# Kernel optimization log

Hardware: AMD Instinct MI355X
Metric: run time of the kernel (lower is better)

Reference implementation:

```python
import jax, jax.numpy as jnp
import numpy as np

N_USERS = 50000
N_ITEMS = 30000
N_ENT = 100000
N_REL = 11          # relations are 1..10; table has N_REL-1 rows
E = 500000          # KG triplets
EI = 1000000        # user-item interaction edges
D = 64              # emb_size (must equal 2*KD for router input)
KD = 32             # FactSemanticEmbedding embedding_dim (complex half-dim)
HID = 64            # GatingRouter hidden (channel)
HOPS = 3            # context_hops
NTH = 3             # hop_threshold N
GAMMA = 0.2


def setup_inputs() -> dict:
    key = jax.random.key(0)
    ks = jax.random.split(key, 24)
    g = lambda i, shape, s=0.1: (jax.random.normal(ks[i], shape) * s).astype(jnp.float32)
    return dict(
        user_embed=g(0, (N_USERS, D)), item_embed=g(1, (N_ITEMS, D)),
        Wq=g(2, (D, D)), Wk=g(3, (D, D)), Wv=g(4, (D, D)),
        ent_real=g(5, (N_ENT, KD)), ent_imag=g(6, (N_ENT, KD)),
        rel_real=g(7, (N_REL - 1, KD)), rel_imag=g(8, (N_REL - 1, KD)),
        fp_W1=g(9, (6 * KD, 2 * KD)), fp_b1=jnp.zeros((2 * KD,), jnp.float32),
        fp_W2=g(10, (2 * KD, 3)), fp_b2=jnp.zeros((3,), jnp.float32),
        rt_W1=g(11, (D, HID)), rt_b1=jnp.zeros((HID,), jnp.float32),
        rt_W2=g(12, (HID, D)), rt_b2=jnp.zeros((D,), jnp.float32),
        relation_emb=g(13, (N_REL - 1, D)),
        user_emb=g(14, (N_USERS, D)), entity_emb=g(15, (N_ENT, D)),
        inter_edge_w=jax.random.uniform(ks[16], (EI,), jnp.float32),
        edge_index=jax.random.randint(ks[17], (2, E), 0, N_ENT),
        edge_type=jax.random.randint(ks[18], (E,), 1, N_REL),
        inter_edge=jnp.stack([jax.random.randint(ks[19], (EI,), 0, N_USERS),
                              jax.random.randint(ks[20], (EI,), 0, N_ITEMS)]),
    )


def _normalize(x):  # F.normalize(dim=-1, eps=1e-8)
    n = jnp.linalg.norm(x, axis=-1, keepdims=True)
    return x / jnp.maximum(n, 1e-8)


def _n2n(x):
    return jnp.nan_to_num(x, nan=0.0, posinf=1e4, neginf=1e-4)


def reference(user_embed, item_embed, Wq, Wk, Wv, ent_real, ent_imag, rel_real,
              rel_imag, fp_W1, fp_b1, fp_W2, fp_b2, rt_W1, rt_b1, rt_W2, rt_b2,
              relation_emb, user_emb, entity_emb, inter_edge_w,
              edge_index, edge_type, inter_edge):
    users, items = inter_edge[0], inter_edge[1]
    # --- AttentionPreferenceMiner (dropout off / eval) ---
    q = (user_embed @ Wq)[users]           # [EI, D]
    k = (item_embed @ Wk)[items]
    v = (item_embed @ Wv)[items]
    scores = (q * k).sum(-1) / jnp.sqrt(jnp.float32(D)) * inter_edge_w
    m = jax.ops.segment_max(scores, users, num_segments=N_USERS)
    ex = jnp.exp(scores - m[users])
    den = jax.ops.segment_sum(ex, users, num_segments=N_USERS)
    alpha = ex / den[users]                # scatter_softmax over users
    cnt_u = jax.ops.segment_sum(jnp.ones_like(scores), users, num_segments=N_USERS)
    user_pref = jax.ops.segment_sum(v * alpha[:, None], users, num_segments=N_USERS)
    user_pref = user_pref / jnp.maximum(cnt_u, 1.0)[:, None]   # scatter_mean
    # --- FactSemanticEmbedding ---
    h, t = edge_index[0], edge_index[1]
    r = edge_type - 1
    hr, hi = ent_real[h], ent_imag[h]
    rr, ri = rel_real[r], rel_imag[r]
    tr, ti = ent_real[t], ent_imag[t]
    feat = jnp.concatenate([hr, hi, rr, ri, tr, ti], axis=-1)  # [E, 6*KD]
    w = jax.nn.softmax(jax.nn.sigmoid(feat @ fp_W1 + fp_b1) @ fp_W2 + fp_b2, axis=-1)
    br = w[:, 0:1] * hr + w[:, 1:2] * rr + w[:, 2:3] * tr
    bi = w[:, 0:1] * hi + w[:, 1:2] * ri + w[:, 2:3] * ti
    fact = jnp.concatenate([br, bi], axis=1)                   # [E, D]
    # --- GatingRouter: sum_j (aligned @ pref^T)[i,j] == aligned @ pref.sum(0) ---
    aligned = jax.nn.sigmoid(fact @ rt_W1 + rt_b1) @ rt_W2 + rt_b2
    omega = (aligned @ user_pref.sum(0)) / jnp.sqrt(jnp.float32(HID))  # [E]
    # --- GraphConv (mess_dropout off) ---
    rel_e = relation_emb[r]                                    # [E, D]
    cnt_h = jax.ops.segment_sum(jnp.ones((E,), omega.dtype), h, num_segments=N_ENT)
    seg_o = jax.ops.segment_sum(omega, h, num_segments=E)      # dim_size=omega.shape[0]
    alpha_g = omega / (seg_o[h] + 1e-8)
    eta = jnp.where(alpha_g > GAMMA, alpha_g, 0.0)
    seg_e = jax.ops.segment_sum(eta, h, num_segments=E)
    eta = eta / (seg_e[h] + 1e-8)
    e_emb, u_emb = entity_emb, user_emb
    ent_res, usr_res = entity_emb, user_emb
    for hop in range(1, HOPS + 1):
        neigh = e_emb[t] * rel_e
        rho = alpha_g if hop < NTH else eta
        e_agg = jax.ops.segment_sum(rho[:, None] * neigh, h, num_segments=N_ENT)
        e_agg = e_agg / jnp.maximum(cnt_h, 1.0)[:, None]       # scatter_mean
        item_agg = inter_edge_w[:, None] * e_emb[items]
        u_agg = jax.ops.segment_sum(item_agg, users, num_segments=N_USERS)
        e_emb = _n2n(_normalize(e_agg))
        u_emb = _n2n(_normalize(u_agg))
        ent_res = ent_res + e_emb
        usr_res = usr_res + u_emb
    return jnp.concatenate([ent_res, usr_res], axis=0)        # [N_ENT+N_USERS, D]
```

## Files before the change

### kernel.cpp

```cpp
#include <hip/hip_runtime.h>
#include <hip/hip_bf16.h>
#include <math.h>

#define N_USERS 50000
#define N_ITEMS 30000
#define N_ENT   100000
#define NE      500000
#define NEI     1000000
#define D       64
#define GAMMA   0.2f

#define UBK ((N_USERS + 255) / 256)
#define HBK ((N_ENT + 255) / 256)
#define PCHUNK 4096

typedef __hip_bfloat16 bf16;

__device__ __forceinline__ float wave_sum(float v) {
    #pragma unroll
    for (int off = 32; off > 0; off >>= 1) v += __shfl_xor(v, off, 64);
    return v;
}

__device__ __forceinline__ float g16_sum(float v) {
    #pragma unroll
    for (int off = 1; off < 16; off <<= 1) v += __shfl_xor(v, off, 64);
    return v;
}

__device__ __forceinline__ float bits2f(unsigned short u) {
    return __uint_as_float(((unsigned)u) << 16);
}

__device__ __forceinline__ unsigned short f2bf_bits(float f) {
    bf16 b = __float2bfloat16(f);
    return *(unsigned short*)&b;
}

__device__ __forceinline__ float sigmoidf(float x) {
    return __fdividef(1.0f, 1.0f + __expf(-x));
}

__device__ __forceinline__ float n2n(float y) {
    if (isnan(y)) return 0.0f;
    if (isinf(y)) return y > 0.0f ? 1e4f : 1e-4f;
    return y;
}

__global__ __launch_bounds__(256) void k_histb(const int* __restrict__ ie,
        const int* __restrict__ eidx, int* __restrict__ bcntU,
        int* __restrict__ bcntH, int UCH) {
    __shared__ int lc[HBK + 1];
    int t = threadIdx.x;
    int b = blockIdx.x;
    for (int i = t; i < HBK + 1; i += 256) lc[i] = 0;
    __syncthreads();
    if (b < UCH) {
        int base = b * PCHUNK;
        #pragma unroll
        for (int i = 0; i < PCHUNK / 256; i++) {
            int e = base + i * 256 + t;
            if (e < NEI) atomicAdd(&lc[ie[e] >> 8], 1);
        }
        __syncthreads();
        for (int i = t; i < UBK; i += 256) if (lc[i]) atomicAdd(&bcntU[i], lc[i]);
    } else {
        int base = (b - UCH) * PCHUNK;
        #pragma unroll
        for (int i = 0; i < PCHUNK / 256; i++) {
            int e = base + i * 256 + t;
            if (e < NE) atomicAdd(&lc[eidx[e] >> 8], 1);
        }
        __syncthreads();
        for (int i = t; i < HBK; i += 256) if (lc[i]) atomicAdd(&bcntH[i], lc[i]);
    }
}

__global__ void k_scanb(const int* __restrict__ bcntU, int* __restrict__ bOffU,
                        int* __restrict__ bcurU, const int* __restrict__ bcntH,
                        int* __restrict__ bOffH, int* __restrict__ bcurH,
                        int* __restrict__ offU, int* __restrict__ offH) {
    __shared__ int sh[512];
    int t = threadIdx.x;
    const int* c; int* o; int* cu; int n; int tot;
    if (blockIdx.x == 0) { c = bcntU; o = bOffU; cu = bcurU; n = UBK; tot = NEI; }
    else                 { c = bcntH; o = bOffH; cu = bcurH; n = HBK; tot = NE; }
    int v = (t < n) ? c[t] : 0;
    sh[t] = v;
    __syncthreads();
    for (int d = 1; d < 512; d <<= 1) {
        int x = (t >= d) ? sh[t - d] : 0;
        __syncthreads();
        sh[t] += x;
        __syncthreads();
    }
    if (t < n) { int ex = sh[t] - v; o[t] = ex; cu[t] = ex; }
    if (t == 0) {
        o[n] = tot;
        if (blockIdx.x == 0) offU[N_USERS] = NEI;
        else                 offH[N_ENT] = NE;
    }
}

__global__ __launch_bounds__(256) void k_part1(const int* __restrict__ ie,
        const float* __restrict__ w, const int* __restrict__ eidx,
        const int* __restrict__ etype, int* __restrict__ bcurU,
        int* __restrict__ bcurH, int2* __restrict__ stIW,
        int* __restrict__ stTR, int UCH) {
    __shared__ int lcnt[HBK + 1];
    __shared__ int lbase[HBK + 1];
    int t = threadIdx.x;
    int b = blockIdx.x;
    for (int i = t; i < HBK + 1; i += 256) lcnt[i] = 0;
    __syncthreads();
    if (b < UCH) {
        int base = b * PCHUNK;
        int bkt[PCHUNK / 256], rnk[PCHUNK / 256];
        #pragma unroll
        for (int i = 0; i < PCHUNK / 256; i++) {
            int e = base + i * 256 + t;
            bkt[i] = -1;
            rnk[i] = 0;
            if (e < NEI) {
                int k = ie[e] >> 8;
                bkt[i] = k;
                rnk[i] = atomicAdd(&lcnt[k], 1);
            }
        }
        __syncthreads();
        for (int i = t; i < UBK; i += 256)
            if (lcnt[i] > 0) lbase[i] = atomicAdd(&bcurU[i], lcnt[i]);
        __syncthreads();
        #pragma unroll
        for (int i = 0; i < PCHUNK / 256; i++) {
            int e = base + i * 256 + t;
            if (bkt[i] >= 0) {
                int pos = lbase[bkt[i]] + rnk[i];
                int ul = ie[e] & 255;
                stIW[pos] = make_int2(ie[NEI + e] | (ul << 24), __float_as_int(w[e]));
            }
        }
    } else {
        int base = (b - UCH) * PCHUNK;
        int bkt[PCHUNK / 256], rnk[PCHUNK / 256];
        #pragma unroll
        for (int i = 0; i < PCHUNK / 256; i++) {
            int e = base + i * 256 + t;
            bkt[i] = -1;
            rnk[i] = 0;
            if (e < NE) {
                int k = eidx[e] >> 8;
                bkt[i] = k;
                rnk[i] = atomicAdd(&lcnt[k], 1);
            }
        }
        __syncthreads();
        for (int i = t; i < HBK; i += 256)
            if (lcnt[i] > 0) lbase[i] = atomicAdd(&bcurH[i], lcnt[i]);
        __syncthreads();
        #pragma unroll
        for (int i = 0; i < PCHUNK / 256; i++) {
            int e = base + i * 256 + t;
            if (bkt[i] >= 0) {
                int pos = lbase[bkt[i]] + rnk[i];
                int hl = eidx[e] & 255;
                stTR[pos] = eidx[NE + e] | ((etype[e] - 1) << 20) | (hl << 24);
            }
        }
    }
}

__global__ __launch_bounds__(256) void k_part2(const int* __restrict__ bOffU,
        const int2* __restrict__ stIW, int* __restrict__ offU,
        int2* __restrict__ csr_itw, const int* __restrict__ bOffH,
        const int* __restrict__ stTR, int* __restrict__ offH,
        int* __restrict__ csr_tr, int UBKc) {
    __shared__ int lcnt[256];
    __shared__ int lcur[256];
    int t = threadIdx.x;
    int b = blockIdx.x;
    lcnt[t] = 0;
    __syncthreads();
    if (b < UBKc) {
        int s = bOffU[b], e = bOffU[b + 1];
        for (int j = s + t; j < e; j += 256)
            atomicAdd(&lcnt[((unsigned)stIW[j].x) >> 24], 1);
        __syncthreads();
        int v = lcnt[t];
        lcur[t] = v;
        __syncthreads();
        for (int d = 1; d < 256; d <<= 1) {
            int x = (t >= d) ? lcur[t - d] : 0;
            __syncthreads();
            lcur[t] += x;
            __syncthreads();
        }
        int base = s + lcur[t] - v;
        int u = (b << 8) + t;
        if (u < N_USERS) offU[u] = base;
        __syncthreads();
        lcur[t] = base;
        __syncthreads();
        for (int j = s + t; j < e; j += 256) {
            int2 r = stIW[j];
            int pos = atomicAdd(&lcur[((unsigned)r.x) >> 24], 1);
            csr_itw[pos] = make_int2(r.x & 0x00FFFFFF, r.y);
        }
    } else {
        int bb = b - UBKc;
        int s = bOffH[bb], e = bOffH[bb + 1];
        for (int j = s + t; j < e; j += 256)
            atomicAdd(&lcnt[((unsigned)stTR[j]) >> 24], 1);
        __syncthreads();
        int v = lcnt[t];
        lcur[t] = v;
        __syncthreads();
        for (int d = 1; d < 256; d <<= 1) {
            int x = (t >= d) ? lcur[t - d] : 0;
            __syncthreads();
            lcur[t] += x;
            __syncthreads();
        }
        int base = s + lcur[t] - v;
        int h = (bb << 8) + t;
        if (h < N_ENT) offH[h] = base;
        __syncthreads();
        lcur[t] = base;
        __syncthreads();
        for (int j = s + t; j < e; j += 256) {
            int r = stTR[j];
            int pos = atomicAdd(&lcur[((unsigned)r) >> 24], 1);
            csr_tr[pos] = r & 0x00FFFFFF;
        }
    }
}

__device__ __forceinline__ void stage_rows2(const float* __restrict__ s0,
                                            const float* __restrict__ s1,
                                            float* At, int row0, int n, int t) {
    #pragma unroll
    for (int half = 0; half < 2; half++) {
        const float* src = half ? s1 : s0;
        int kofs = half ? 32 : 0;
        #pragma unroll
        for (int fi = t, it = 0; it < 2; fi += 256, it++) {
            int row = fi >> 3;
            int k4 = (fi & 7) << 2;
            float4 v = make_float4(0.f, 0.f, 0.f, 0.f);
            if (row0 + row < n) v = *(const float4*)&src[(size_t)(row0 + row) * 32 + k4];
            At[(kofs + k4 + 0) * 64 + row] = v.x;
            At[(kofs + k4 + 1) * 64 + row] = v.y;
            At[(kofs + k4 + 2) * 64 + row] = v.z;
            At[(kofs + k4 + 3) * 64 + row] = v.w;
        }
    }
}

__device__ __forceinline__ void stage_rows1(const float* __restrict__ src,
                                            float* At, int row0, int n, int t) {
    #pragma unroll
    for (int fi = t, it = 0; it < 4; fi += 256, it++) {
        int row = fi >> 4;
        int k4 = (fi & 15) << 2;
        float4 v = make_float4(0.f, 0.f, 0.f, 0.f);
        if (row0 + row < n) v = *(const float4*)&src[(size_t)(row0 + row) * 64 + k4];
        At[(k4 + 0) * 64 + row] = v.x;
        At[(k4 + 1) * 64 + row] = v.y;
        At[(k4 + 2) * 64 + row] = v.z;
        At[(k4 + 3) * 64 + row] = v.w;
    }
}

__global__ __launch_bounds__(256) void k_proj(const float* __restrict__ I,
        const float* __restrict__ Wk, const float* __restrict__ Wv,
        const float* __restrict__ UE, const float* __restrict__ Wq,
        bf16* __restrict__ IkB, float* __restrict__ Iv, float* __restrict__ Uq, int IB) {
    __shared__ float At[64 * 64];
    int t = threadIdx.x;
    int b = blockIdx.x;
    int lane = t & 63;
    int wv = __builtin_amdgcn_readfirstlane(t >> 6);
    if (b < IB) {
        int row0 = b << 6;
        stage_rows1(I, At, row0, N_ITEMS, t);
        __syncthreads();
        const float* Wb = ((wv >> 1) ? Wv : Wk) + (wv & 1) * 32;
        float acc[32];
        #pragma unroll
        for (int c = 0; c < 32; c++) acc[c] = 0.f;
        for (int k = 0; k < 64; k++) {
            float a = At[k * 64 + lane];
            const float* wr = Wb + k * 64;
            #pragma unroll
            for (int c4 = 0; c4 < 8; c4++) {
                float4 w4 = *(const float4*)&wr[c4 * 4];
                acc[c4 * 4 + 0] += a * w4.x;
                acc[c4 * 4 + 1] += a * w4.y;
                acc[c4 * 4 + 2] += a * w4.z;
                acc[c4 * 4 + 3] += a * w4.w;
            }
        }
        int row = row0 + lane;
        if (row < N_ITEMS) {
            if (wv >> 1) {
                float* dst = Iv + (size_t)row * 64 + (wv & 1) * 32;
                #pragma unroll
                for (int c4 = 0; c4 < 8; c4++)
                    *(float4*)&dst[c4 * 4] = make_float4(acc[c4*4], acc[c4*4+1], acc[c4*4+2], acc[c4*4+3]);
            } else {
                bf16* dst = IkB + (size_t)row * 64 + (wv & 1) * 32;
                #pragma unroll
                for (int c4 = 0; c4 < 8; c4++) {
                    ushort4 s;
                    s.x = f2bf_bits(acc[c4 * 4 + 0]);
                    s.y = f2bf_bits(acc[c4 * 4 + 1]);
                    s.z = f2bf_bits(acc[c4 * 4 + 2]);
                    s.w = f2bf_bits(acc[c4 * 4 + 3]);
                    *(ushort4*)&dst[c4 * 4] = s;
                }
            }
        }
    } else {
        int row0 = (b - IB) << 6;
        stage_rows1(UE, At, row0, N_USERS, t);
        __syncthreads();
        const float* Wb = Wq + wv * 16;
        float acc[16];
        #pragma unroll
        for (int c = 0; c < 16; c++) acc[c] = 0.f;
        for (int k = 0; k < 64; k++) {
            float a = At[k * 64 + lane];
            const float* wr = Wb + k * 64;
            #pragma unroll
            for (int c4 = 0; c4 < 4; c4++) {
                float4 w4 = *(const float4*)&wr[c4 * 4];
                acc[c4 * 4 + 0] += a * w4.x;
                acc[c4 * 4 + 1] += a * w4.y;
                acc[c4 * 4 + 2] += a * w4.z;
                acc[c4 * 4 + 3] += a * w4.w;
            }
        }
        int row = row0 + lane;
        if (row < N_USERS) {
            float* dst = Uq + (size_t)row * 64 + wv * 16;
            #pragma unroll
            for (int c4 = 0; c4 < 4; c4++)
                *(float4*)&dst[c4 * 4] = make_float4(acc[c4*4], acc[c4*4+1], acc[c4*4+2], acc[c4*4+3]);
        }
    }
}

__global__ __launch_bounds__(256) void k_userAB(const int* __restrict__ offU,
                        const int2* __restrict__ itw,
                        const float* __restrict__ Uq, const bf16* __restrict__ IkB,
                        float* __restrict__ exA, float* __restrict__ c, int n) {
    int u = (blockIdx.x * blockDim.x + threadIdx.x) >> 6;
    int lane = threadIdx.x & 63;
    if (u >= n) return;
    int s = offU[u], e = offU[u + 1];
    if (s == e) return;
    int l = lane & 15, g = lane >> 4;
    float4 qv = *(const float4*)&Uq[(size_t)u * D + l * 4];
    const char* kbase = (const char*)IkB;
    unsigned dby = (unsigned)(l << 3);
    float den = 0.f;
    for (int j0 = s; j0 < e; j0 += 8) {
        int jA = j0 + g, jB = jA + 4;
        bool vA = jA < e, vB = jB < e;
        int2 iA = itw[vA ? jA : s];
        int2 iB = itw[vB ? jB : s];
        ushort4 kA = *(const ushort4*)(kbase + (((unsigned)iA.x) << 7) + dby);
        ushort4 kB = *(const ushort4*)(kbase + (((unsigned)iB.x) << 7) + dby);
        float dA = qv.x * bits2f(kA.x) + qv.y * bits2f(kA.y) +
                   qv.z * bits2f(kA.z) + qv.w * bits2f(kA.w);
        float dB = qv.x * bits2f(kB.x) + qv.y * bits2f(kB.y) +
                   qv.z * bits2f(kB.z) + qv.w * bits2f(kB.w);
        #pragma unroll
        for (int off = 1; off < 16; off <<= 1) {
            dA += __shfl_xor(dA, off, 64);
            dB += __shfl_xor(dB, off, 64);
        }
        float eAv = vA ? __expf(dA * 0.125f * __int_as_float(iA.y)) : 0.f;
        float eBv = vB ? __expf(dB * 0.125f * __int_as_float(iB.y)) : 0.f;
        den += eAv + eBv;
        if (vA && l == 0) exA[jA] = eAv;
        if (vB && l == 0) exA[jB] = eBv;
    }
    den += __shfl_xor(den, 16, 64);
    den += __shfl_xor(den, 32, 64);
    float inv = __fdividef(1.0f, den * (float)(e - s));
    asm volatile("s_waitcnt vmcnt(0)" ::: "memory");
    for (int j = s + lane; j < e; j += 64)
        atomicAdd(&c[itw[j].x], exA[j] * inv);
}

__global__ void k_pdense(const float* __restrict__ c, const float* __restrict__ Iv,
                         float* __restrict__ p, int n) {
    int lane = threadIdx.x & 63;
    int gw = blockIdx.x * 4 + (threadIdx.x >> 6);
    int nw = gridDim.x * 4;
    float acc = 0.f;
    for (int i = gw; i < n; i += nw) acc += c[i] * Iv[(size_t)i * D + lane];
    __shared__ float red[256];
    red[threadIdx.x] = acc;
    __syncthreads();
    if (threadIdx.x < 64) {
        float s = red[threadIdx.x] + red[threadIdx.x + 64] + red[threadIdx.x + 128] + red[threadIdx.x + 192];
        atomicAdd(&p[threadIdx.x], s);
    }
}

__global__ __launch_bounds__(256) void k_entabx(const float* __restrict__ er,
        const float* __restrict__ ei, const float* __restrict__ fpW1,
        const float* __restrict__ rr, const float* __restrict__ ri,
        const float* __restrict__ rtW1, const float* __restrict__ rtW2,
        const float* __restrict__ rt_b2, const float* __restrict__ p,
        float* __restrict__ EH, float* __restrict__ ET, float* __restrict__ PHI,
        float* __restrict__ RR1, float* __restrict__ PSI,
        float* __restrict__ v2, float* __restrict__ cb, int EB) {
    __shared__ float At[64 * 64];
    int b = blockIdx.x;
    int t = threadIdx.x;
    if (b < EB) {
        int row0 = b << 6;
        stage_rows2(er, ei, At, row0, N_ENT, t);
        __syncthreads();
        int lane = t & 63;
        int wv = __builtin_amdgcn_readfirstlane(t >> 6);
        const float* Wb = fpW1 + ((wv >> 1) ? (128 * 64) : 0) + (wv & 1) * 32;
        float acc[32];
        #pragma unroll
        for (int c = 0; c < 32; c++) acc[c] = 0.f;
        for (int k = 0; k < 64; k++) {
            float a = At[k * 64 + lane];
            const float* wr = Wb + k * 64;
            #pragma unroll
            for (int c4 = 0; c4 < 8; c4++) {
                float4 w4 = *(const float4*)&wr[c4 * 4];
                acc[c4 * 4 + 0] += a * w4.x;
                acc[c4 * 4 + 1] += a * w4.y;
                acc[c4 * 4 + 2] += a * w4.z;
                acc[c4 * 4 + 3] += a * w4.w;
            }
        }
        int row = row0 + lane;
        if (row < N_ENT) {
            float* dst = ((wv >> 1) ? ET : EH) + (size_t)row * 64 + (wv & 1) * 32;
            #pragma unroll
            for (int c4 = 0; c4 < 8; c4++)
                *(float4*)&dst[c4 * 4] = make_float4(acc[c4*4], acc[c4*4+1], acc[c4*4+2], acc[c4*4+3]);
        }
    } else if (b < 2 * EB) {
        int row0 = (b - EB) << 6;
        stage_rows2(er, ei, At, row0, N_ENT, t);
        __syncthreads();
        int lane = t & 63;
        int wv = __builtin_amdgcn_readfirstlane(t >> 6);
        const float* Wb = rtW1 + wv * 16;
        float acc[16];
        #pragma unroll
        for (int c = 0; c < 16; c++) acc[c] = 0.f;
        for (int k = 0; k < 64; k++) {
            float a = At[k * 64 + lane];
            const float* wr = Wb + k * 64;
            #pragma unroll
            for (int c4 = 0; c4 < 4; c4++) {
                float4 w4 = *(const float4*)&wr[c4 * 4];
                acc[c4 * 4 + 0] += a * w4.x;
                acc[c4 * 4 + 1] += a * w4.y;
                acc[c4 * 4 + 2] += a * w4.z;
                acc[c4 * 4 + 3] += a * w4.w;
            }
        }
        int row = row0 + lane;
        if (row < N_ENT) {
            float* dst = PHI + (size_t)row * 64 + wv * 16;
            #pragma unroll
            for (int c4 = 0; c4 < 4; c4++)
                *(float4*)&dst[c4 * 4] = make_float4(acc[c4*4], acc[c4*4+1], acc[c4*4+2], acc[c4*4+3]);
        }
    } else if (b == 2 * EB) {
        if (t < 64) {
            int lane = t;
            for (int r = 0; r < 10; r++) {
                float a = 0.f, bb = 0.f;
                for (int k = 0; k < 32; k++) {
                    float sr = rr[r * 32 + k], si = ri[r * 32 + k];
                    a  += sr * fpW1[(64 + k) * D + lane] + si * fpW1[(96 + k) * D + lane];
                    bb += sr * rtW1[k * D + lane] + si * rtW1[(32 + k) * D + lane];
                }
                RR1[r * D + lane] = a;
                PSI[r * D + lane] = bb;
            }
        }
    } else {
        if (t < 64) {
            int j = t;
            float acc = 0.f;
            #pragma unroll
            for (int k = 0; k < D; k++) acc += rtW2[j * D + k] * p[k];
            v2[j] = acc;
            float cc = rt_b2[j] * p[j];
            cc = wave_sum(cc);
            if (j == 0) cb[0] = cc;
        }
    }
}

__global__ __launch_bounds__(256) void k_omega(const int* __restrict__ offH,
                          const int* __restrict__ csr_tr,
                          const float* __restrict__ EH, const float* __restrict__ ET,
                          const float* __restrict__ PHI, const float* __restrict__ PSI,
                          const float* __restrict__ RR1, const float* __restrict__ fp_b1,
                          const float* __restrict__ fpW2, const float* __restrict__ fp_b2,
                          const float* __restrict__ rt_b1, const float* __restrict__ v2,
                          const float* __restrict__ cb,
                          float* __restrict__ omg, int2* __restrict__ pa,
                          int2* __restrict__ pe,
                          const float* __restrict__ src_emb, bf16* __restrict__ eA,
                          int OB, int n) {
    int b = blockIdx.x;
    if (b >= OB) {
        int base = (b - OB) * 1024 + threadIdx.x * 4;
        float4 v = *(const float4*)&src_emb[base];
        ushort4 s;
        s.x = f2bf_bits(v.x); s.y = f2bf_bits(v.y);
        s.z = f2bf_bits(v.z); s.w = f2bf_bits(v.w);
        *(ushort4*)&eA[base] = s;
        return;
    }
    int h = (b * blockDim.x + threadIdx.x) >> 6;
    int lane = threadIdx.x & 63;
    if (h >= n) return;
    int s = offH[h], e = offH[h + 1];
    if (s == e) return;
    int l = lane & 15, g = lane >> 4;
    int d0 = l * 4;
    float4 ehh = *(const float4*)&EH[(size_t)h * D + d0];
    float4 b1 = *(const float4*)&fp_b1[d0];
    ehh.x += b1.x; ehh.y += b1.y; ehh.z += b1.z; ehh.w += b1.w;
    float f0[4], f1[4], f2[4];
    #pragma unroll
    for (int cc4 = 0; cc4 < 4; cc4++) {
        f0[cc4] = fpW2[(d0 + cc4) * 3 + 0];
        f1[cc4] = fpW2[(d0 + cc4) * 3 + 1];
        f2[cc4] = fpW2[(d0 + cc4) * 3 + 2];
    }
    float b20 = fp_b2[0], b21 = fp_b2[1], b22 = fp_b2[2];
    float4 phh = *(const float4*)&PHI[(size_t)h * D + d0];
    float4 rb = *(const float4*)&rt_b1[d0];
    float4 vv = *(const float4*)&v2[d0];
    float cc = cb[0];
    float so = 0.f;
    for (int j0 = s; j0 < e; j0 += 8) {
        int jA = j0 + g, jB = jA + 4;
        bool vA = jA < e, vB = jB < e;
        int pkA = csr_tr[vA ? jA : s];
        int pkB = csr_tr[vB ? jB : s];
        int tA = pkA & 0xFFFFF, rA = pkA >> 20;
        int tB = pkB & 0xFFFFF, rB = pkB >> 20;
        float4 etA = *(const float4*)&ET[(size_t)tA * D + d0];
        float4 etB = *(const float4*)&ET[(size_t)tB * D + d0];
        float4 ptA = *(const float4*)&PHI[(size_t)tA * D + d0];
        float4 ptB = *(const float4*)&PHI[(size_t)tB * D + d0];
        float4 rrA = *(const float4*)&RR1[rA * D + d0];
        float4 rrB = *(const float4*)&RR1[rB * D + d0];
        float4 psA = *(const float4*)&PSI[rA * D + d0];
        float4 psB = *(const float4*)&PSI[rB * D + d0];
        float zA0 = sigmoidf(ehh.x + rrA.x + etA.x);
        float zA1 = sigmoidf(ehh.y + rrA.y + etA.y);
        float zA2 = sigmoidf(ehh.z + rrA.z + etA.z);
        float zA3 = sigmoidf(ehh.w + rrA.w + etA.w);
        float zB0 = sigmoidf(ehh.x + rrB.x + etB.x);
        float zB1 = sigmoidf(ehh.y + rrB.y + etB.y);
        float zB2 = sigmoidf(ehh.z + rrB.z + etB.z);
        float zB3 = sigmoidf(ehh.w + rrB.w + etB.w);
        float v[6];
        v[0] = zA0 * f0[0] + zA1 * f0[1] + zA2 * f0[2] + zA3 * f0[3];
        v[1] = zA0 * f1[0] + zA1 * f1[1] + zA2 * f1[2] + zA3 * f1[3];
        v[2] = zA0 * f2[0] + zA1 * f2[1] + zA2 * f2[2] + zA3 * f2[3];
        v[3] = zB0 * f0[0] + zB1 * f0[1] + zB2 * f0[2] + zB3 * f0[3];
        v[4] = zB0 * f1[0] + zB1 * f1[1] + zB2 * f1[2] + zB3 * f1[3];
        v[5] = zB0 * f2[0] + zB1 * f2[1] + zB2 * f2[2] + zB3 * f2[3];
        #pragma unroll
        for (int off = 1; off < 16; off <<= 1) {
            #pragma unroll
            for (int q = 0; q < 6; q++) v[q] += __shfl_xor(v[q], off, 64);
        }
        float a0 = v[0] + b20, a1 = v[1] + b21, a2 = v[2] + b22;
        float mx = fmaxf(a0, fmaxf(a1, a2));
        float e0 = __expf(a0 - mx), e1 = __expf(a1 - mx), e2 = __expf(a2 - mx);
        float isum = __fdividef(1.0f, e0 + e1 + e2);
        float WA0 = e0 * isum, WA1 = e1 * isum, WA2 = e2 * isum;
        a0 = v[3] + b20; a1 = v[4] + b21; a2 = v[5] + b22;
        mx = fmaxf(a0, fmaxf(a1, a2));
        e0 = __expf(a0 - mx); e1 = __expf(a1 - mx); e2 = __expf(a2 - mx);
        isum = __fdividef(1.0f, e0 + e1 + e2);
        float WB0 = e0 * isum, WB1 = e1 * isum, WB2 = e2 * isum;
        float svA = sigmoidf(WA0 * phh.x + WA1 * psA.x + WA2 * ptA.x + rb.x) * vv.x
                  + sigmoidf(WA0 * phh.y + WA1 * psA.y + WA2 * ptA.y + rb.y) * vv.y
                  + sigmoidf(WA0 * phh.z + WA1 * psA.z + WA2 * ptA.z + rb.z) * vv.z
                  + sigmoidf(WA0 * phh.w + WA1 * psA.w + WA2 * ptA.w + rb.w) * vv.w;
        float svB = sigmoidf(WB0 * phh.x + WB1 * psB.x + WB2 * ptB.x + rb.x) * vv.x
                  + sigmoidf(WB0 * phh.y + WB1 * psB.y + WB2 * ptB.y + rb.y) * vv.y
                  + sigmoidf(WB0 * phh.z + WB1 * psB.z + WB2 * ptB.z + rb.z) * vv.z
                  + sigmoidf(WB0 * phh.w + WB1 * psB.w + WB2 * ptB.w + rb.w) * vv.w;
        #pragma unroll
        for (int off = 1; off < 16; off <<= 1) {
            svA += __shfl_xor(svA, off, 64);
            svB += __shfl_xor(svB, off, 64);
        }
        float omA = (svA + cc) * 0.125f;
        float omB = (svB + cc) * 0.125f;
        if (vA) { if (l == 0) omg[jA] = omA; so += omA; }
        if (vB) { if (l == 0) omg[jB] = omB; so += omB; }
    }
    so += __shfl_xor(so, 16, 64);
    so += __shfl_xor(so, 32, 64);
    float invO = __fdividef(1.0f, so + 1e-8f);
    asm volatile("s_waitcnt vmcnt(0)" ::: "memory");
    float se = 0.f;
    for (int j = s + lane; j < e; j += 64) {
        float a = omg[j] * invO;
        pa[j] = make_int2(csr_tr[j], __float_as_int(a));
        se += (a > GAMMA) ? a : 0.0f;
    }
    se = wave_sum(se);
    float invE = __fdividef(1.0f, se + 1e-8f);
    for (int j = s + lane; j < e; j += 64) {
        float a = omg[j] * invO;
        pe[j] = make_int2(csr_tr[j], __float_as_int(((a > GAMMA) ? a : 0.0f) * invE));
    }
}

__global__ __launch_bounds__(256) void k_hop(const int* __restrict__ offH,
                      const int2* __restrict__ rt,
                      const float* __restrict__ rel,
                      const int* __restrict__ offU, const int2* __restrict__ itw,
                      const bf16* __restrict__ ecur, bf16* __restrict__ enxt,
                      const float* __restrict__ initE, const float* __restrict__ initU,
                      float* __restrict__ outE, float* __restrict__ outU,
                      int init, int EB) {
    int b = blockIdx.x;
    int lane = threadIdx.x & 63;
    int l = lane & 15, g = lane >> 4;
    int d0 = l * 4;
    const char* ebase = (const char*)ecur;
    unsigned dby = (unsigned)(d0 << 1);
    if (b < EB) {
        int gw = b * 4 + (threadIdx.x >> 6);
        if (gw >= N_ENT) return;
        int s = offH[gw], e = offH[gw + 1];
        float a0 = 0.f, a1 = 0.f, a2 = 0.f, a3 = 0.f;
        for (int j0 = s; j0 < e; j0 += 8) {
            int jA = j0 + g, jB = jA + 4;
            bool vA = jA < e, vB = jB < e;
            int2 pA = rt[vA ? jA : s];
            int2 pB = rt[vB ? jB : s];
            float rhA = vA ? __int_as_float(pA.y) : 0.f;
            float rhB = vB ? __int_as_float(pB.y) : 0.f;
            unsigned tA = (unsigned)pA.x & 0xFFFFFu; int rA = pA.x >> 20;
            unsigned tB = (unsigned)pB.x & 0xFFFFFu; int rB = pB.x >> 20;
            ushort4 evA = *(const ushort4*)(ebase + (tA << 7) + dby);
            ushort4 evB = *(const ushort4*)(ebase + (tB << 7) + dby);
            float4 rlA = *(const float4*)&rel[rA * D + d0];
            float4 rlB = *(const float4*)&rel[rB * D + d0];
            a0 += rhA * bits2f(evA.x) * rlA.x;
            a1 += rhA * bits2f(evA.y) * rlA.y;
            a2 += rhA * bits2f(evA.z) * rlA.z;
            a3 += rhA * bits2f(evA.w) * rlA.w;
            a0 += rhB * bits2f(evB.x) * rlB.x;
            a1 += rhB * bits2f(evB.y) * rlB.y;
            a2 += rhB * bits2f(evB.z) * rlB.z;
            a3 += rhB * bits2f(evB.w) * rlB.w;
        }
        a0 += __shfl_xor(a0, 16, 64); a0 += __shfl_xor(a0, 32, 64);
        a1 += __shfl_xor(a1, 16, 64); a1 += __shfl_xor(a1, 32, 64);
        a2 += __shfl_xor(a2, 16, 64); a2 += __shfl_xor(a2, 32, 64);
        a3 += __shfl_xor(a3, 16, 64); a3 += __shfl_xor(a3, 32, 64);
        float invd = __fdividef(1.0f, fmaxf((float)(e - s), 1.0f));
        a0 *= invd; a1 *= invd; a2 *= invd; a3 *= invd;
        float ss = a0 * a0 + a1 * a1 + a2 * a2 + a3 * a3;
        ss = g16_sum(ss);
        float nrm = fmaxf(sqrtf(ss), 1e-8f);
        float innrm = __fdividef(1.0f, nrm);
        float y0 = n2n(a0 * innrm), y1 = n2n(a1 * innrm), y2 = n2n(a2 * innrm), y3 = n2n(a3 * innrm);
        if (g == 0) {
            ushort4 st;
            st.x = f2bf_bits(y0); st.y = f2bf_bits(y1); st.z = f2bf_bits(y2); st.w = f2bf_bits(y3);
            *(ushort4*)&enxt[(size_t)gw * D + d0] = st;
            size_t o = (size_t)gw * D + d0;
            float4 prev;
            if (init) prev = *(const float4*)&initE[o];
            else      prev = *(const float4*)&outE[o];
            *(float4*)&outE[o] = make_float4(prev.x + y0, prev.y + y1, prev.z + y2, prev.w + y3);
        }
    } else {
        int gw = (b - EB) * 4 + (threadIdx.x >> 6);
        if (gw >= N_USERS) return;
        int s = offU[gw], e = offU[gw + 1];
        float a0 = 0.f, a1 = 0.f, a2 = 0.f, a3 = 0.f;
        for (int j0 = s; j0 < e; j0 += 8) {
            int jA = j0 + g, jB = jA + 4;
            bool vA = jA < e, vB = jB < e;
            int2 iA = itw[vA ? jA : s];
            int2 iB = itw[vB ? jB : s];
            float wA = vA ? __int_as_float(iA.y) : 0.f;
            float wB = vB ? __int_as_float(iB.y) : 0.f;
            ushort4 evA = *(const ushort4*)(ebase + (((unsigned)iA.x) << 7) + dby);
            ushort4 evB = *(const ushort4*)(ebase + (((unsigned)iB.x) << 7) + dby);
            a0 += wA * bits2f(evA.x) + wB * bits2f(evB.x);
            a1 += wA * bits2f(evA.y) + wB * bits2f(evB.y);
            a2 += wA * bits2f(evA.z) + wB * bits2f(evB.z);
            a3 += wA * bits2f(evA.w) + wB * bits2f(evB.w);
        }
        a0 += __shfl_xor(a0, 16, 64); a0 += __shfl_xor(a0, 32, 64);
        a1 += __shfl_xor(a1, 16, 64); a1 += __shfl_xor(a1, 32, 64);
        a2 += __shfl_xor(a2, 16, 64); a2 += __shfl_xor(a2, 32, 64);
        a3 += __shfl_xor(a3, 16, 64); a3 += __shfl_xor(a3, 32, 64);
        float ss = a0 * a0 + a1 * a1 + a2 * a2 + a3 * a3;
        ss = g16_sum(ss);
        float nrm = fmaxf(sqrtf(ss), 1e-8f);
        float innrm = __fdividef(1.0f, nrm);
        float y0 = n2n(a0 * innrm), y1 = n2n(a1 * innrm), y2 = n2n(a2 * innrm), y3 = n2n(a3 * innrm);
        if (g == 0) {
            size_t o = (size_t)gw * D + d0;
            float4 prev;
            if (init) prev = *(const float4*)&initU[o];
            else      prev = *(const float4*)&outU[o];
            *(float4*)&outU[o] = make_float4(prev.x + y0, prev.y + y1, prev.z + y2, prev.w + y3);
        }
    }
}

extern "C" void kernel_launch(void* const* d_in, const int* in_sizes, int n_in,
                              void* d_out, int out_size, void* d_ws, size_t ws_size,
                              hipStream_t stream) {
    const float* user_embed = (const float*)d_in[0];
    const float* item_embed = (const float*)d_in[1];
    const float* Wq = (const float*)d_in[2];
    const float* Wk = (const float*)d_in[3];
    const float* Wv = (const float*)d_in[4];
    const float* ent_real = (const float*)d_in[5];
    const float* ent_imag = (const float*)d_in[6];
    const float* rel_real = (const float*)d_in[7];
    const float* rel_imag = (const float*)d_in[8];
    const float* fp_W1 = (const float*)d_in[9];
    const float* fp_b1 = (const float*)d_in[10];
    const float* fp_W2 = (const float*)d_in[11];
    const float* fp_b2 = (const float*)d_in[12];
    const float* rt_W1 = (const float*)d_in[13];
    const float* rt_b1 = (const float*)d_in[14];
    const float* rt_W2 = (const float*)d_in[15];
    const float* rt_b2 = (const float*)d_in[16];
    const float* relation_emb = (const float*)d_in[17];
    const float* user_emb = (const float*)d_in[18];
    const float* entity_emb = (const float*)d_in[19];
    const float* inter_edge_w = (const float*)d_in[20];
    const int* edge_index = (const int*)d_in[21];
    const int* edge_type = (const int*)d_in[22];
    const int* inter_edge = (const int*)d_in[23];
    float* out = (float*)d_out;

    float* W = (float*)d_ws;
    size_t off = 0;
    auto alloc = [&](size_t n) { float* r = W + off; off += n; return r; };
    float* omg    = alloc(NE);
    float* exA    = alloc(NEI);
    float* c      = alloc(N_ITEMS);
    float* p      = alloc(64);
    float* v2     = alloc(64);
    float* cb     = alloc(64);
    float* RR1    = alloc(10 * D);
    float* PSI    = alloc(10 * D);
    off = (off + 3) & ~(size_t)3;
    int* IW = (int*)(W + off);
    size_t ioff = 0;
    auto ialloc = [&](size_t n) { int* r = IW + ioff; ioff += n; return r; };
    int2* csr_itw = (int2*)ialloc(2 * (size_t)NEI);
    int2* pa      = (int2*)ialloc(2 * (size_t)NE);
    int2* pe      = (int2*)ialloc(2 * (size_t)NE);
    int* csr_tr = ialloc(NE);
    int* offU   = ialloc(N_USERS + 1);
    int* offH   = ialloc(N_ENT + 1);
    int* bcntU  = ialloc(UBK);
    int* bcntH  = ialloc(HBK);
    int* bOffU  = ialloc(UBK + 1);
    int* bOffH  = ialloc(HBK + 1);
    int* bcurU  = ialloc(UBK);
    int* bcurH  = ialloc(HBK);
    off += ioff;
    off = (off + 3) & ~(size_t)3;
    float* U = W + off;
    int2* stIW = (int2*)U;
    int*  stTR = (int*)U + 2 * (size_t)NEI;
    bf16*  IkB = (bf16*)U;
    float* Iv  = U + (size_t)N_ITEMS * 32;
    float* Uq  = Iv + (size_t)N_ITEMS * D;
    float* EH  = U;
    float* ET  = U + (size_t)N_ENT * D;
    float* PHI = U + 2 * (size_t)N_ENT * D;
    bf16*  eA  = (bf16*)(U + 3 * (size_t)N_ENT * D);
    bf16* eB = (bf16*)U;

    const int UCH = (NEI + PCHUNK - 1) / PCHUNK;
    const int HCH = (NE + PCHUNK - 1) / PCHUNK;
    const int IB = (N_ITEMS + 63) / 64;
    const int UB = (N_USERS + 63) / 64;
    const int EB = (N_ENT + 63) / 64;
    const int OB = (N_ENT + 3) / 4;
    const int CB = (N_ENT * D) / 1024;
    const int HE = (N_ENT + 3) / 4;
    const int HU = (N_USERS + 3) / 4;

    hipMemsetAsync(bcntU, 0, (UBK + HBK) * 4, stream);
    hipMemsetAsync(c, 0, (N_ITEMS + 64) * 4, stream);
    k_histb<<<UCH + HCH, 256, 0, stream>>>(inter_edge, edge_index, bcntU, bcntH, UCH);
    k_scanb<<<2, 512, 0, stream>>>(bcntU, bOffU, bcurU, bcntH, bOffH, bcurH, offU, offH);
    k_part1<<<UCH + HCH, 256, 0, stream>>>(inter_edge, inter_edge_w, edge_index,
                                           edge_type, bcurU, bcurH, stIW, stTR, UCH);
    k_part2<<<UBK + HBK, 256, 0, stream>>>(bOffU, stIW, offU, csr_itw,
                                           bOffH, stTR, offH, csr_tr, UBK);

    k_proj<<<IB + UB, 256, 0, stream>>>(item_embed, Wk, Wv, user_embed, Wq,
                                        IkB, Iv, Uq, IB);
    k_userAB<<<(N_USERS + 3) / 4, 256, 0, stream>>>(offU, csr_itw, Uq, IkB, exA, c, N_USERS);
    k_pdense<<<64, 256, 0, stream>>>(c, Iv, p, N_ITEMS);

    k_entabx<<<2 * EB + 2, 256, 0, stream>>>(ent_real, ent_imag, fp_W1, rel_real, rel_imag,
                                             rt_W1, rt_W2, rt_b2, p, EH, ET, PHI,
                                             RR1, PSI, v2, cb, EB);
    k_omega<<<OB + CB, 256, 0, stream>>>(offH, csr_tr, EH, ET, PHI, PSI, RR1,
                                         fp_b1, fp_W2, fp_b2, rt_b1, v2, cb,
                                         omg, pa, pe, entity_emb, eA, OB, N_ENT);

    bf16* ecur = eA;
    bf16* enxt = eB;
    for (int hop = 1; hop <= 3; hop++) {
        const int2* rt = (hop < 3) ? pa : pe;
        int init = (hop == 1) ? 1 : 0;
        k_hop<<<HE + HU, 256, 0, stream>>>(offH, rt, relation_emb,
                                           offU, csr_itw, ecur, enxt,
                                           entity_emb, user_emb,
                                           out, out + (size_t)N_ENT * D, init, HE);
        bf16* tmp = ecur; ecur = enxt; enxt = tmp;
    }
}
```

Baseline: 741.9 us.

## Parallelize omega per edge and shrink hop kernels to 16-lane groups per node

The omega computation was one wave per head entity looping over its edges. It is now an edge-parallel kernel that uses a new per-edge head index array written during CSR build, plus a separate segment-normalization kernel run by 16-lane groups. The hop aggregation kernels now give each entity or user a 16-lane group instead of a full wave, which removes the cross-group shuffles and the idle lanes on low-degree nodes. This adds an extra launch and extra reads of head rows (EH/PHI per edge). Each group now works through its edge list sequentially, so nodes with many edges take longer.

```diff
diff --git a/kernel.cpp b/kernel.cpp
--- a/kernel.cpp
+++ b/kernel.cpp
@@ -174,7 +174,7 @@
         const int2* __restrict__ stIW, int* __restrict__ offU,
         int2* __restrict__ csr_itw, const int* __restrict__ bOffH,
         const int* __restrict__ stTR, int* __restrict__ offH,
-        int* __restrict__ csr_tr, int UBKc) {
+        int* __restrict__ csr_tr, int* __restrict__ csr_h, int UBKc) {
     __shared__ int lcnt[256];
     __shared__ int lcur[256];
     int t = threadIdx.x;
@@ -231,6 +231,7 @@
             int r = stTR[j];
             int pos = atomicAdd(&lcur[((unsigned)r) >> 24], 1);
             csr_tr[pos] = r & 0x00FFFFFF;
+            csr_h[pos] = (bb << 8) + (int)(((unsigned)r) >> 24);
         }
     }
 }
@@ -507,21 +508,19 @@
     }
 }
 
-__global__ __launch_bounds__(256) void k_omega(const int* __restrict__ offH,
-                          const int* __restrict__ csr_tr,
+__global__ __launch_bounds__(256) void k_omegaE(const int* __restrict__ csr_tr,
+                          const int* __restrict__ csr_h,
                           const float* __restrict__ EH, const float* __restrict__ ET,
                           const float* __restrict__ PHI, const float* __restrict__ PSI,
                           const float* __restrict__ RR1, const float* __restrict__ fp_b1,
                           const float* __restrict__ fpW2, const float* __restrict__ fp_b2,
                           const float* __restrict__ rt_b1, const float* __restrict__ v2,
-                          const float* __restrict__ cb,
-                          float* __restrict__ omg, int2* __restrict__ pa,
-                          int2* __restrict__ pe,
+                          const float* __restrict__ cb, float* __restrict__ omg,
                           const float* __restrict__ src_emb, bf16* __restrict__ eA,
-                          int OB, int n) {
+                          int NB) {
     int b = blockIdx.x;
-    if (b >= OB) {
-        int base = (b - OB) * 1024 + threadIdx.x * 4;
+    if (b >= NB) {
+        int base = (b - NB) * 1024 + threadIdx.x * 4;
         float4 v = *(const float4*)&src_emb[base];
         ushort4 s;
         s.x = f2bf_bits(v.x); s.y = f2bf_bits(v.y);
@@ -529,105 +528,112 @@
         *(ushort4*)&eA[base] = s;
         return;
     }
-    int h = (b * blockDim.x + threadIdx.x) >> 6;
-    int lane = threadIdx.x & 63;
+    int grp = threadIdx.x >> 4;
+    int l = threadIdx.x & 15;
+    int d0 = l * 4;
+    int jA = b * 32 + grp;
+    int jB = jA + 16;
+    float4 b1 = *(const float4*)&fp_b1[d0];
+    float4 rb = *(const float4*)&rt_b1[d0];
+    float4 vv = *(const float4*)&v2[d0];
+    float cc = cb[0];
+    float f0[4], f1[4], f2[4];
+    #pragma unroll
+    for (int c4 = 0; c4 < 4; c4++) {
+        f0[c4] = fpW2[(d0 + c4) * 3 + 0];
+        f1[c4] = fpW2[(d0 + c4) * 3 + 1];
+        f2[c4] = fpW2[(d0 + c4) * 3 + 2];
+    }
+    float b20 = fp_b2[0], b21 = fp_b2[1], b22 = fp_b2[2];
+    int pkA = csr_tr[jA], pkB = csr_tr[jB];
+    int hA = csr_h[jA], hB = csr_h[jB];
+    int tA = pkA & 0xFFFFF, rA = pkA >> 20;
+    int tB = pkB & 0xFFFFF, rB = pkB >> 20;
+    float4 ehA = *(const float4*)&EH[(size_t)hA * D + d0];
+    float4 ehB = *(const float4*)&EH[(size_t)hB * D + d0];
+    float4 phA = *(const float4*)&PHI[(size_t)hA * D + d0];
+    float4 phB = *(const float4*)&PHI[(size_t)hB * D + d0];
+    float4 etA = *(const float4*)&ET[(size_t)tA * D + d0];
+    float4 etB = *(const float4*)&ET[(size_t)tB * D + d0];
+    float4 ptA = *(const float4*)&PHI[(size_t)tA * D + d0];
+    float4 ptB = *(const float4*)&PHI[(size_t)tB * D + d0];
+    float4 rrA = *(const float4*)&RR1[rA * D + d0];
+    float4 rrB = *(const float4*)&RR1[rB * D + d0];
+    float4 psA = *(const float4*)&PSI[rA * D + d0];
+    float4 psB = *(const float4*)&PSI[rB * D + d0];
+    ehA.x += b1.x; ehA.y += b1.y; ehA.z += b1.z; ehA.w += b1.w;
+    ehB.x += b1.x; ehB.y += b1.y; ehB.z += b1.z; ehB.w += b1.w;
+    float zA0 = sigmoidf(ehA.x + rrA.x + etA.x);
+    float zA1 = sigmoidf(ehA.y + rrA.y + etA.y);
+    float zA2 = sigmoidf(ehA.z + rrA.z + etA.z);
+    float zA3 = sigmoidf(ehA.w + rrA.w + etA.w);
+    float zB0 = sigmoidf(ehB.x + rrB.x + etB.x);
+    float zB1 = sigmoidf(ehB.y + rrB.y + etB.y);
+    float zB2 = sigmoidf(ehB.z + rrB.z + etB.z);
+    float zB3 = sigmoidf(ehB.w + rrB.w + etB.w);
+    float v[6];
+    v[0] = zA0 * f0[0] + zA1 * f0[1] + zA2 * f0[2] + zA3 * f0[3];
+    v[1] = zA0 * f1[0] + zA1 * f1[1] + zA2 * f1[2] + zA3 * f1[3];
+    v[2] = zA0 * f2[0] + zA1 * f2[1] + zA2 * f2[2] + zA3 * f2[3];
+    v[3] = zB0 * f0[0] + zB1 * f0[1] + zB2 * f0[2] + zB3 * f0[3];
+    v[4] = zB0 * f1[0] + zB1 * f1[1] + zB2 * f1[2] + zB3 * f1[3];
+    v[5] = zB0 * f2[0] + zB1 * f2[1] + zB2 * f2[2] + zB3 * f2[3];
+    #pragma unroll
+    for (int off = 1; off < 16; off <<= 1) {
+        #pragma unroll
+        for (int q = 0; q < 6; q++) v[q] += __shfl_xor(v[q], off, 64);
+    }
+    float a0 = v[0] + b20, a1 = v[1] + b21, a2 = v[2] + b22;
+    float mx = fmaxf(a0, fmaxf(a1, a2));
+    float e0 = __expf(a0 - mx), e1 = __expf(a1 - mx), e2 = __expf(a2 - mx);
+    float isum = __fdividef(1.0f, e0 + e1 + e2);
+    float WA0 = e0 * isum, WA1 = e1 * isum, WA2 = e2 * isum;
+    a0 = v[3] + b20; a1 = v[4] + b21; a2 = v[5] + b22;
+    mx = fmaxf(a0, fmaxf(a1, a2));
+    e0 = __expf(a0 - mx); e1 = __expf(a1 - mx); e2 = __expf(a2 - mx);
+    isum = __fdividef(1.0f, e0 + e1 + e2);
+    float WB0 = e0 * isum, WB1 = e1 * isum, WB2 = e2 * isum;
+    float svA = sigmoidf(WA0 * phA.x + WA1 * psA.x + WA2 * ptA.x + rb.x) * vv.x
+              + sigmoidf(WA0 * phA.y + WA1 * psA.y + WA2 * ptA.y + rb.y) * vv.y
+              + sigmoidf(WA0 * phA.z + WA1 * psA.z + WA2 * ptA.z + rb.z) * vv.z
+              + sigmoidf(WA0 * phA.w + WA1 * psA.w + WA2 * ptA.w + rb.w) * vv.w;
+    float svB = sigmoidf(WB0 * phB.x + WB1 * psB.x + WB2 * ptB.x + rb.x) * vv.x
+              + sigmoidf(WB0 * phB.y + WB1 * psB.y + WB2 * ptB.y + rb.y) * vv.y
+              + sigmoidf(WB0 * phB.z + WB1 * psB.z + WB2 * ptB.z + rb.z) * vv.z
+              + sigmoidf(WB0 * phB.w + WB1 * psB.w + WB2 * ptB.w + rb.w) * vv.w;
+    #pragma unroll
+    for (int off = 1; off < 16; off <<= 1) {
+        svA += __shfl_xor(svA, off, 64);
+        svB += __shfl_xor(svB, off, 64);
+    }
+    if (l == 0) {
+        omg[jA] = (svA + cc) * 0.125f;
+        omg[jB] = (svB + cc) * 0.125f;
+    }
+}
+
+__global__ __launch_bounds__(256) void k_omegaS(const int* __restrict__ offH,
+                          const int* __restrict__ csr_tr,
+                          const float* __restrict__ omg,
+                          int2* __restrict__ pa, int2* __restrict__ pe, int n) {
+    int h = (blockIdx.x * 256 + threadIdx.x) >> 4;
+    int l = threadIdx.x & 15;
     if (h >= n) return;
     int s = offH[h], e = offH[h + 1];
     if (s == e) return;
-    int l = lane & 15, g = lane >> 4;
-    int d0 = l * 4;
-    float4 ehh = *(const float4*)&EH[(size_t)h * D + d0];
-    float4 b1 = *(const float4*)&fp_b1[d0];
-    ehh.x += b1.x; ehh.y += b1.y; ehh.z += b1.z; ehh.w += b1.w;
-    float f0[4], f1[4], f2[4];
-    #pragma unroll
-    for (int cc4 = 0; cc4 < 4; cc4++) {
-        f0[cc4] = fpW2[(d0 + cc4) * 3 + 0];
-        f1[cc4] = fpW2[(d0 + cc4) * 3 + 1];
-        f2[cc4] = fpW2[(d0 + cc4) * 3 + 2];
-    }
-    float b20 = fp_b2[0], b21 = fp_b2[1], b22 = fp_b2[2];
-    float4 phh = *(const float4*)&PHI[(size_t)h * D + d0];
-    float4 rb = *(const float4*)&rt_b1[d0];
-    float4 vv = *(const float4*)&v2[d0];
-    float cc = cb[0];
     float so = 0.f;
-    for (int j0 = s; j0 < e; j0 += 8) {
-        int jA = j0 + g, jB = jA + 4;
-        bool vA = jA < e, vB = jB < e;
-        int pkA = csr_tr[vA ? jA : s];
-        int pkB = csr_tr[vB ? jB : s];
-        int tA = pkA & 0xFFFFF, rA = pkA >> 20;
-        int tB = pkB & 0xFFFFF, rB = pkB >> 20;
-        float4 etA = *(const float4*)&ET[(size_t)tA * D + d0];
-        float4 etB = *(const float4*)&ET[(size_t)tB * D + d0];
-        float4 ptA = *(const float4*)&PHI[(size_t)tA * D + d0];
-        float4 ptB = *(const float4*)&PHI[(size_t)tB * D + d0];
-        float4 rrA = *(const float4*)&RR1[rA * D + d0];
-        float4 rrB = *(const float4*)&RR1[rB * D + d0];
-        float4 psA = *(const float4*)&PSI[rA * D + d0];
-        float4 psB = *(const float4*)&PSI[rB * D + d0];
-        float zA0 = sigmoidf(ehh.x + rrA.x + etA.x);
-        float zA1 = sigmoidf(ehh.y + rrA.y + etA.y);
-        float zA2 = sigmoidf(ehh.z + rrA.z + etA.z);
-        float zA3 = sigmoidf(ehh.w + rrA.w + etA.w);
-        float zB0 = sigmoidf(ehh.x + rrB.x + etB.x);
-        float zB1 = sigmoidf(ehh.y + rrB.y + etB.y);
-        float zB2 = sigmoidf(ehh.z + rrB.z + etB.z);
-        float zB3 = sigmoidf(ehh.w + rrB.w + etB.w);
-        float v[6];
-        v[0] = zA0 * f0[0] + zA1 * f0[1] + zA2 * f0[2] + zA3 * f0[3];
-        v[1] = zA0 * f1[0] + zA1 * f1[1] + zA2 * f1[2] + zA3 * f1[3];
-        v[2] = zA0 * f2[0] + zA1 * f2[1] + zA2 * f2[2] + zA3 * f2[3];
-        v[3] = zB0 * f0[0] + zB1 * f0[1] + zB2 * f0[2] + zB3 * f0[3];
-        v[4] = zB0 * f1[0] + zB1 * f1[1] + zB2 * f1[2] + zB3 * f1[3];
-        v[5] = zB0 * f2[0] + zB1 * f2[1] + zB2 * f2[2] + zB3 * f2[3];
-        #pragma unroll
-        for (int off = 1; off < 16; off <<= 1) {
-            #pragma unroll
-            for (int q = 0; q < 6; q++) v[q] += __shfl_xor(v[q], off, 64);
-        }
-        float a0 = v[0] + b20, a1 = v[1] + b21, a2 = v[2] + b22;
-        float mx = fmaxf(a0, fmaxf(a1, a2));
-        float e0 = __expf(a0 - mx), e1 = __expf(a1 - mx), e2 = __expf(a2 - mx);
-        float isum = __fdividef(1.0f, e0 + e1 + e2);
-        float WA0 = e0 * isum, WA1 = e1 * isum, WA2 = e2 * isum;
-        a0 = v[3] + b20; a1 = v[4] + b21; a2 = v[5] + b22;
-        mx = fmaxf(a0, fmaxf(a1, a2));
-        e0 = __expf(a0 - mx); e1 = __expf(a1 - mx); e2 = __expf(a2 - mx);
-        isum = __fdividef(1.0f, e0 + e1 + e2);
-        float WB0 = e0 * isum, WB1 = e1 * isum, WB2 = e2 * isum;
-        float svA = sigmoidf(WA0 * phh.x + WA1 * psA.x + WA2 * ptA.x + rb.x) * vv.x
-                  + sigmoidf(WA0 * phh.y + WA1 * psA.y + WA2 * ptA.y + rb.y) * vv.y
-                  + sigmoidf(WA0 * phh.z + WA1 * psA.z + WA2 * ptA.z + rb.z) * vv.z
-                  + sigmoidf(WA0 * phh.w + WA1 * psA.w + WA2 * ptA.w + rb.w) * vv.w;
-        float svB = sigmoidf(WB0 * phh.x + WB1 * psB.x + WB2 * ptB.x + rb.x) * vv.x
-                  + sigmoidf(WB0 * phh.y + WB1 * psB.y + WB2 * ptB.y + rb.y) * vv.y
-                  + sigmoidf(WB0 * phh.z + WB1 * psB.z + WB2 * ptB.z + rb.z) * vv.z
-                  + sigmoidf(WB0 * phh.w + WB1 * psB.w + WB2 * ptB.w + rb.w) * vv.w;
-        #pragma unroll
-        for (int off = 1; off < 16; off <<= 1) {
-            svA += __shfl_xor(svA, off, 64);
-            svB += __shfl_xor(svB, off, 64);
-        }
-        float omA = (svA + cc) * 0.125f;
-        float omB = (svB + cc) * 0.125f;
-        if (vA) { if (l == 0) omg[jA] = omA; so += omA; }
-        if (vB) { if (l == 0) omg[jB] = omB; so += omB; }
-    }
-    so += __shfl_xor(so, 16, 64);
-    so += __shfl_xor(so, 32, 64);
+    for (int j = s + l; j < e; j += 16) so += omg[j];
+    so = g16_sum(so);
     float invO = __fdividef(1.0f, so + 1e-8f);
-    asm volatile("s_waitcnt vmcnt(0)" ::: "memory");
     float se = 0.f;
-    for (int j = s + lane; j < e; j += 64) {
+    for (int j = s + l; j < e; j += 16) {
         float a = omg[j] * invO;
         pa[j] = make_int2(csr_tr[j], __float_as_int(a));
         se += (a > GAMMA) ? a : 0.0f;
     }
-    se = wave_sum(se);
+    se = g16_sum(se);
     float invE = __fdividef(1.0f, se + 1e-8f);
-    for (int j = s + lane; j < e; j += 64) {
+    for (int j = s + l; j < e; j += 16) {
         float a = omg[j] * invO;
         pe[j] = make_int2(csr_tr[j], __float_as_int(((a > GAMMA) ? a : 0.0f) * invE));
     }
@@ -640,24 +646,23 @@
                       const bf16* __restrict__ ecur, bf16* __restrict__ enxt,
                       const float* __restrict__ initE, const float* __restrict__ initU,
                       float* __restrict__ outE, float* __restrict__ outU,
-                      int init, int EB) {
+                      int init, int EB2) {
     int b = blockIdx.x;
-    int lane = threadIdx.x & 63;
-    int l = lane & 15, g = lane >> 4;
+    int l = threadIdx.x & 15;
     int d0 = l * 4;
     const char* ebase = (const char*)ecur;
     unsigned dby = (unsigned)(d0 << 1);
-    if (b < EB) {
-        int gw = b * 4 + (threadIdx.x >> 6);
+    if (b < EB2) {
+        int gw = (b * 256 + threadIdx.x) >> 4;
         if (gw >= N_ENT) return;
         int s = offH[gw], e = offH[gw + 1];
         float a0 = 0.f, a1 = 0.f, a2 = 0.f, a3 = 0.f;
-        for (int j0 = s; j0 < e; j0 += 8) {
-            int jA = j0 + g, jB = jA + 4;
-            bool vA = jA < e, vB = jB < e;
-            int2 pA = rt[vA ? jA : s];
-            int2 pB = rt[vB ? jB : s];
-            float rhA = vA ? __int_as_float(pA.y) : 0.f;
+        for (int j0 = s; j0 < e; j0 += 2) {
+            int jB = j0 + 1;
+            bool vB = jB < e;
+            int2 pA = rt[j0];
+            int2 pB = rt[vB ? jB : j0];
+            float rhA = __int_as_float(pA.y);
             float rhB = vB ? __int_as_float(pB.y) : 0.f;
             unsigned tA = (unsigned)pA.x & 0xFFFFFu; int rA = pA.x >> 20;
             unsigned tB = (unsigned)pB.x & 0xFFFFFu; int rB = pB.x >> 20;
@@ -674,10 +679,6 @@
             a2 += rhB * bits2f(evB.z) * rlB.z;
             a3 += rhB * bits2f(evB.w) * rlB.w;
         }
-        a0 += __shfl_xor(a0, 16, 64); a0 += __shfl_xor(a0, 32, 64);
-        a1 += __shfl_xor(a1, 16, 64); a1 += __shfl_xor(a1, 32, 64);
-        a2 += __shfl_xor(a2, 16, 64); a2 += __shfl_xor(a2, 32, 64);
-        a3 += __shfl_xor(a3, 16, 64); a3 += __shfl_xor(a3, 32, 64);
         float invd = __fdividef(1.0f, fmaxf((float)(e - s), 1.0f));
         a0 *= invd; a1 *= invd; a2 *= invd; a3 *= invd;
         float ss = a0 * a0 + a1 * a1 + a2 * a2 + a3 * a3;
@@ -685,27 +686,25 @@
         float nrm = fmaxf(sqrtf(ss), 1e-8f);
         float innrm = __fdividef(1.0f, nrm);
         float y0 = n2n(a0 * innrm), y1 = n2n(a1 * innrm), y2 = n2n(a2 * innrm), y3 = n2n(a3 * innrm);
-        if (g == 0) {
-            ushort4 st;
-            st.x = f2bf_bits(y0); st.y = f2bf_bits(y1); st.z = f2bf_bits(y2); st.w = f2bf_bits(y3);
-            *(ushort4*)&enxt[(size_t)gw * D + d0] = st;
-            size_t o = (size_t)gw * D + d0;
-            float4 prev;
-            if (init) prev = *(const float4*)&initE[o];
-            else      prev = *(const float4*)&outE[o];
-            *(float4*)&outE[o] = make_float4(prev.x + y0, prev.y + y1, prev.z + y2, prev.w + y3);
-        }
+        ushort4 st;
+        st.x = f2bf_bits(y0); st.y = f2bf_bits(y1); st.z = f2bf_bits(y2); st.w = f2bf_bits(y3);
+        *(ushort4*)&enxt[(size_t)gw * D + d0] = st;
+        size_t o = (size_t)gw * D + d0;
+        float4 prev;
+        if (init) prev = *(const float4*)&initE[o];
+        else      prev = *(const float4*)&outE[o];
+        *(float4*)&outE[o] = make_float4(prev.x + y0, prev.y + y1, prev.z + y2, prev.w + y3);
     } else {
-        int gw = (b - EB) * 4 + (threadIdx.x >> 6);
+        int gw = ((b - EB2) * 256 + threadIdx.x) >> 4;
         if (gw >= N_USERS) return;
         int s = offU[gw], e = offU[gw + 1];
         float a0 = 0.f, a1 = 0.f, a2 = 0.f, a3 = 0.f;
-        for (int j0 = s; j0 < e; j0 += 8) {
-            int jA = j0 + g, jB = jA + 4;
-            bool vA = jA < e, vB = jB < e;
-            int2 iA = itw[vA ? jA : s];
-            int2 iB = itw[vB ? jB : s];
-            float wA = vA ? __int_as_float(iA.y) : 0.f;
+        for (int j0 = s; j0 < e; j0 += 2) {
+            int jB = j0 + 1;
+            bool vB = jB < e;
+            int2 iA = itw[j0];
+            int2 iB = itw[vB ? jB : j0];
+            float wA = __int_as_float(iA.y);
             float wB = vB ? __int_as_float(iB.y) : 0.f;
             ushort4 evA = *(const ushort4*)(ebase + (((unsigned)iA.x) << 7) + dby);
             ushort4 evB = *(const ushort4*)(ebase + (((unsigned)iB.x) << 7) + dby);
@@ -714,22 +713,16 @@
             a2 += wA * bits2f(evA.z) + wB * bits2f(evB.z);
             a3 += wA * bits2f(evA.w) + wB * bits2f(evB.w);
         }
-        a0 += __shfl_xor(a0, 16, 64); a0 += __shfl_xor(a0, 32, 64);
-        a1 += __shfl_xor(a1, 16, 64); a1 += __shfl_xor(a1, 32, 64);
-        a2 += __shfl_xor(a2, 16, 64); a2 += __shfl_xor(a2, 32, 64);
-        a3 += __shfl_xor(a3, 16, 64); a3 += __shfl_xor(a3, 32, 64);
         float ss = a0 * a0 + a1 * a1 + a2 * a2 + a3 * a3;
         ss = g16_sum(ss);
         float nrm = fmaxf(sqrtf(ss), 1e-8f);
         float innrm = __fdividef(1.0f, nrm);
         float y0 = n2n(a0 * innrm), y1 = n2n(a1 * innrm), y2 = n2n(a2 * innrm), y3 = n2n(a3 * innrm);
-        if (g == 0) {
-            size_t o = (size_t)gw * D + d0;
-            float4 prev;
-            if (init) prev = *(const float4*)&initU[o];
-            else      prev = *(const float4*)&outU[o];
-            *(float4*)&outU[o] = make_float4(prev.x + y0, prev.y + y1, prev.z + y2, prev.w + y3);
-        }
+        size_t o = (size_t)gw * D + d0;
+        float4 prev;
+        if (init) prev = *(const float4*)&initU[o];
+        else      prev = *(const float4*)&outU[o];
+        *(float4*)&outU[o] = make_float4(prev.x + y0, prev.y + y1, prev.z + y2, prev.w + y3);
     }
 }
 
@@ -781,6 +774,7 @@
     int2* pa      = (int2*)ialloc(2 * (size_t)NE);
     int2* pe      = (int2*)ialloc(2 * (size_t)NE);
     int* csr_tr = ialloc(NE);
+    int* csr_h  = ialloc(NE);
     int* offU   = ialloc(N_USERS + 1);
     int* offH   = ialloc(N_ENT + 1);
     int* bcntU  = ialloc(UBK);
@@ -808,10 +802,11 @@
     const int IB = (N_ITEMS + 63) / 64;
     const int UB = (N_USERS + 63) / 64;
     const int EB = (N_ENT + 63) / 64;
-    const int OB = (N_ENT + 3) / 4;
+    const int OEB = NE / 32;
     const int CB = (N_ENT * D) / 1024;
-    const int HE = (N_ENT + 3) / 4;
-    const int HU = (N_USERS + 3) / 4;
+    const int SB = (N_ENT + 15) / 16;
+    const int HE2 = (N_ENT + 15) / 16;
+    const int HU2 = (N_USERS + 15) / 16;
 
     hipMemsetAsync(bcntU, 0, (UBK + HBK) * 4, stream);
     hipMemsetAsync(c, 0, (N_ITEMS + 64) * 4, stream);
@@ -820,7 +815,7 @@
     k_part1<<<UCH + HCH, 256, 0, stream>>>(inter_edge, inter_edge_w, edge_index,
                                            edge_type, bcurU, bcurH, stIW, stTR, UCH);
     k_part2<<<UBK + HBK, 256, 0, stream>>>(bOffU, stIW, offU, csr_itw,
-                                           bOffH, stTR, offH, csr_tr, UBK);
+                                           bOffH, stTR, offH, csr_tr, csr_h, UBK);
 
     k_proj<<<IB + UB, 256, 0, stream>>>(item_embed, Wk, Wv, user_embed, Wq,
                                         IkB, Iv, Uq, IB);
@@ -830,19 +825,20 @@
     k_entabx<<<2 * EB + 2, 256, 0, stream>>>(ent_real, ent_imag, fp_W1, rel_real, rel_imag,
                                              rt_W1, rt_W2, rt_b2, p, EH, ET, PHI,
                                              RR1, PSI, v2, cb, EB);
-    k_omega<<<OB + CB, 256, 0, stream>>>(offH, csr_tr, EH, ET, PHI, PSI, RR1,
-                                         fp_b1, fp_W2, fp_b2, rt_b1, v2, cb,
-                                         omg, pa, pe, entity_emb, eA, OB, N_ENT);
+    k_omegaE<<<OEB + CB, 256, 0, stream>>>(csr_tr, csr_h, EH, ET, PHI, PSI, RR1,
+                                           fp_b1, fp_W2, fp_b2, rt_b1, v2, cb,
+                                           omg, entity_emb, eA, OEB);
+    k_omegaS<<<SB, 256, 0, stream>>>(offH, csr_tr, omg, pa, pe, N_ENT);
 
     bf16* ecur = eA;
     bf16* enxt = eB;
     for (int hop = 1; hop <= 3; hop++) {
         const int2* rt = (hop < 3) ? pa : pe;
         int init = (hop == 1) ? 1 : 0;
-        k_hop<<<HE + HU, 256, 0, stream>>>(offH, rt, relation_emb,
-                                           offU, csr_itw, ecur, enxt,
-                                           entity_emb, user_emb,
-                                           out, out + (size_t)N_ENT * D, init, HE);
+        k_hop<<<HE2 + HU2, 256, 0, stream>>>(offH, rt, relation_emb,
+                                             offU, csr_itw, ecur, enxt,
+                                             entity_emb, user_emb,
+                                             out, out + (size_t)N_ENT * D, init, HE2);
         bf16* tmp = ecur; ecur = enxt; enxt = tmp;
     }
 }
```

New measurement: 650.0 us. 1.14x faster.
